# Kernel tuning notes

Hardware: AMD Instinct MI355X
Metric: run time of the kernel (lower is better)

Reference implementation:

```python
import jax, jax.numpy as jnp
import numpy as np

INV_TEMPERATURE = 0.125  # 1/sqrt(head_dim=64)


def setup_inputs() -> dict:
    key = jax.random.key(0)
    kq, kk, kv, kp, km = jax.random.split(key, 5)
    B, H, S, D = 8, 8, 2048, 64
    q = jax.random.normal(kq, (B, H, S, D), dtype=jnp.float32)
    k = jax.random.normal(kk, (B, H, S, D), dtype=jnp.float32)
    v = jax.random.normal(kv, (B, H, S, D), dtype=jnp.float32)
    pos_scores = jax.random.normal(kp, (1, H, S, S), dtype=jnp.float32)
    mask = jax.random.uniform(km, (1, 1, S, S), dtype=jnp.float32)
    return {"q": q, "k": k, "v": v, "pos_scores": pos_scores, "mask": mask}


def reference(q, k, v, pos_scores, mask):
    # sim = (q k^T) * inv_temp + pos_scores, then multiplicative mask
    sim = jnp.einsum('bhid,bhjd->bhij', q, k) * INV_TEMPERATURE
    sim = mask * (sim + pos_scores)
    attn = jax.nn.softmax(sim, axis=-1)
    out = jnp.einsum('bhij,bhjd->bhid', attn, v)
    return out
```

## Files before the change

### kernel.cpp

```cpp
#include <hip/hip_runtime.h>

constexpr int SEQ = 2048;
constexpr int HD  = 64;
constexpr int NH  = 8;
constexpr int NB  = 8;
constexpr int BM  = 64;
constexpr int BN  = 64;
constexpr int KST = 72;
constexpr float INV_T = 0.125f;
constexpr float LOG2E = 1.4426950408889634f;

typedef __attribute__((ext_vector_type(8))) short bf16x8;
typedef __attribute__((ext_vector_type(8))) short s16x8;
typedef __attribute__((ext_vector_type(4))) short s16x4;
typedef __attribute__((ext_vector_type(4))) float f32x4;
typedef __attribute__((ext_vector_type(4))) unsigned u32x4;

__device__ __forceinline__ short f2bf(float f) {
  unsigned u = __builtin_bit_cast(unsigned, f);
  u += 0x7fffu + ((u >> 16) & 1u);
  return (short)(u >> 16);
}
__device__ __forceinline__ float bf2f(short s) {
  unsigned u = ((unsigned)(unsigned short)s) << 16;
  return __builtin_bit_cast(float, u);
}
__device__ __forceinline__ float fast_exp2(float x) {
#if __has_builtin(__builtin_amdgcn_exp2f)
  return __builtin_amdgcn_exp2f(x);
#else
  return exp2f(x);
#endif
}

__global__ __launch_bounds__(256)
void prep_kv(const float* __restrict__ k, const float* __restrict__ v,
             unsigned short* __restrict__ kb, unsigned short* __restrict__ vt)
{
  __shared__ unsigned short t[HD * KST];
  const int bh = blockIdx.y, jt = blockIdx.x, tid = threadIdx.x;
  const size_t base = (size_t)bh * SEQ * HD + (size_t)jt * BN * HD;

  {
    const float* kp = k + base + 16 * tid;
    unsigned short ko[16];
    for (int e = 0; e < 4; ++e) {
      f32x4 x = *(const f32x4*)(kp + 4 * e);
      for (int c = 0; c < 4; ++c) ko[4 * e + c] = (unsigned short)f2bf(x[c]);
    }
    *(s16x8*)(kb + base + 16 * tid)     = *(const s16x8*)&ko[0];
    *(s16x8*)(kb + base + 16 * tid + 8) = *(const s16x8*)&ko[8];
  }
  {
    const float* vp = v + base + 16 * tid;
    const int j = tid >> 2, d0 = (tid & 3) * 16;
    for (int e = 0; e < 4; ++e) {
      f32x4 x = *(const f32x4*)(vp + 4 * e);
      for (int c = 0; c < 4; ++c) t[(d0 + 4 * e + c) * KST + j] = (unsigned short)f2bf(x[c]);
    }
  }
  __syncthreads();
  {
    const int d = tid >> 2, ch = tid & 3;
    const size_t ob = (size_t)bh * HD * SEQ + (size_t)d * SEQ + jt * BN + ch * 16;
    *(s16x8*)(vt + ob)     = *(const s16x8*)&t[d * KST + ch * 16];
    *(s16x8*)(vt + ob + 8) = *(const s16x8*)&t[d * KST + ch * 16 + 8];
  }
}

__global__ __launch_bounds__(256)
void prep_pack(const float* __restrict__ pos, const float* __restrict__ mask,
               unsigned* __restrict__ pk)
{
  const int w  = blockIdx.x * 256 + threadIdx.x;
  const int lq = w & 15;
  const int i  = (w >> 4) & 2047;
  const int jh = w >> 15;
  const int jt = jh & 31, h = jh >> 5;
  u32x4 o;
  for (int sub = 0; sub < 4; ++sub) {
    const int j = jt * 64 + sub * 16 + lq;
    float m = mask[(size_t)i * SEQ + j];
    float p = pos[((size_t)h * SEQ + i) * SEQ + j];
    unsigned mb = (unsigned)(unsigned short)f2bf(m * LOG2E);
    unsigned pb = (unsigned)(unsigned short)f2bf(m * p * LOG2E);
    o[sub] = (mb << 16) | pb;
  }
  *(u32x4*)(pk + (size_t)4 * w) = o;
}

__global__ __launch_bounds__(256, 8)
void attn_main(const float* __restrict__ q, const unsigned short* __restrict__ kb,
               const unsigned short* __restrict__ vt, const unsigned* __restrict__ pk,
               float* __restrict__ out)
{
  __shared__ unsigned short lds_k[BN * KST];
  __shared__ unsigned short lds_v[HD * KST];

  const int bh = blockIdx.y, h = bh & (NH - 1);
  const int i0 = blockIdx.x * BM;
  const int tid = threadIdx.x, wave = tid >> 6, lane = tid & 63;
  const int quad = lane >> 4, lq = lane & 15;

  bf16x8 aq[2];
  {
    const float* qp = q + ((size_t)bh * SEQ + i0 + wave * 16 + lq) * HD + quad * 8;
    for (int k0 = 0; k0 < 2; ++k0) {
      f32x4 x = *(const f32x4*)(qp + k0 * 32);
      f32x4 y = *(const f32x4*)(qp + k0 * 32 + 4);
      for (int c = 0; c < 4; ++c) {
        aq[k0][c]     = f2bf(x[c] * INV_T);
        aq[k0][4 + c] = f2bf(y[c] * INV_T);
      }
    }
  }

  f32x4 oacc[4];
  for (int d = 0; d < 4; ++d) oacc[d] = (f32x4){0.f, 0.f, 0.f, 0.f};
  float lrun[4] = {0.f, 0.f, 0.f, 0.f};

  const int lw = (tid >> 3) * KST + (tid & 7) * 8;
  const unsigned short* kgb = kb + (size_t)bh * SEQ * HD + 8 * tid;
  const unsigned short* vgb = vt + (size_t)bh * HD * SEQ + (tid >> 3) * SEQ + (tid & 7) * 8;
  const unsigned* mpb = pk + ((((size_t)h * 32) * SEQ + (i0 + wave * 16 + quad * 4)) * 16 + lq) * 4;

  for (int jt = 0; jt < SEQ / BN; ++jt) {
    __syncthreads();
    s16x8 kx0 = *(const s16x8*)(kgb + jt * 4096);
    s16x8 kx1 = *(const s16x8*)(kgb + jt * 4096 + 2048);
    s16x8 vx0 = *(const s16x8*)(vgb + jt * 64);
    s16x8 vx1 = *(const s16x8*)(vgb + jt * 64 + 32 * SEQ);
    *(s16x8*)&lds_k[lw]            = kx0;
    *(s16x8*)&lds_k[lw + 32 * KST] = kx1;
    *(s16x8*)&lds_v[lw]            = vx0;
    *(s16x8*)&lds_v[lw + 32 * KST] = vx1;
    __syncthreads();

    f32x4 sa[4];
    for (int s = 0; s < 4; ++s) sa[s] = (f32x4){0.f, 0.f, 0.f, 0.f};
    for (int k0 = 0; k0 < 2; ++k0)
      for (int s = 0; s < 4; ++s) {
        bf16x8 bk = *(const bf16x8*)&lds_k[(s * 16 + lq) * KST + k0 * 32 + quad * 8];
        sa[s] = __builtin_amdgcn_mfma_f32_16x16x32_bf16(aq[k0], bk, sa[s], 0, 0, 0);
      }
    __syncthreads();

    const unsigned* mp = mpb + (size_t)jt * (SEQ * 64);
    for (int r = 0; r < 4; ++r) {
      u32x4 u = *(const u32x4*)(mp + r * 64);
      float ps = 0.f;
      for (int s = 0; s < 4; ++s) {
        float mf = __builtin_bit_cast(float, u[s] & 0xffff0000u);
        float mq = __builtin_bit_cast(float, u[s] << 16);
        float p  = fast_exp2(fmaf(mf, sa[s][r], mq));
        unsigned pu = __builtin_bit_cast(unsigned, p);
        lds_k[wave * (16 * KST) + (quad * 4 + r) * KST + s * 16 + lq] = (unsigned short)(pu >> 16);
        ps += __builtin_bit_cast(float, pu & 0xffff0000u);
      }
      for (int off = 1; off < 16; off <<= 1) ps += __shfl_xor(ps, off);
      lrun[r] += ps;
    }
    asm volatile("s_waitcnt lgkmcnt(0)" ::: "memory");

    for (int k0 = 0; k0 < 2; ++k0) {
      bf16x8 ap = *(const bf16x8*)&lds_k[wave * (16 * KST) + lq * KST + k0 * 32 + quad * 8];
      for (int d = 0; d < 4; ++d) {
        bf16x8 bv = *(const bf16x8*)&lds_v[(d * 16 + lq) * KST + k0 * 32 + quad * 8];
        oacc[d] = __builtin_amdgcn_mfma_f32_16x16x32_bf16(ap, bv, oacc[d], 0, 0, 0);
      }
    }
  }

  for (int r = 0; r < 4; ++r) {
    const float inv = 1.0f / lrun[r];
    float* orow = out + ((size_t)bh * SEQ + i0 + wave * 16 + quad * 4 + r) * HD + lq;
    for (int d = 0; d < 4; ++d) orow[d * 16] = oacc[d][r] * inv;
  }
}

__global__ __launch_bounds__(256, 2)
void attn_fused(const float* __restrict__ q, const float* __restrict__ kk,
                const float* __restrict__ vv, const float* __restrict__ pos,
                const float* __restrict__ mask, float* __restrict__ out)
{
  __shared__ short lds_k[BN * KST];
  __shared__ short lds_v[HD * KST];
  __shared__ short lds_p[4][16 * KST];
  const int bh = blockIdx.y, h = bh & (NH - 1);
  const int i0 = blockIdx.x * BM;
  const int tid = threadIdx.x, wave = tid >> 6, lane = tid & 63;
  const int quad = lane >> 4, lq = lane & 15;
  bf16x8 aq[2];
  {
    const float* qp = q + ((size_t)bh * SEQ + i0 + wave * 16 + lq) * HD + quad * 8;
    for (int k0 = 0; k0 < 2; ++k0) {
      f32x4 x = *(const f32x4*)(qp + k0 * 32);
      f32x4 y = *(const f32x4*)(qp + k0 * 32 + 4);
      for (int j = 0; j < 4; ++j) { aq[k0][j] = f2bf(x[j] * INV_T); aq[k0][4 + j] = f2bf(y[j] * INV_T); }
    }
  }
  f32x4 oacc[4];
  for (int d = 0; d < 4; ++d) oacc[d] = (f32x4){0.f, 0.f, 0.f, 0.f};
  float mrun[4] = {-INFINITY, -INFINITY, -INFINITY, -INFINITY};
  float lrun[4] = {0.f, 0.f, 0.f, 0.f};
  const size_t kvbase = (size_t)bh * SEQ * HD;
  for (int jt = 0; jt < SEQ / BN; ++jt) {
    const int j0 = jt * BN;
    __syncthreads();
    for (int e = 0; e < 4; ++e) {
      int idx = e * 256 + tid, j = idx >> 4, d4 = (idx & 15) << 2;
      f32x4 kf = *(const f32x4*)(kk + kvbase + (size_t)(j0 + j) * HD + d4);
      s16x4 ks;
      for (int c = 0; c < 4; ++c) ks[c] = f2bf(kf[c]);
      *(s16x4*)&lds_k[j * KST + d4] = ks;
      f32x4 vf = *(const f32x4*)(vv + kvbase + (size_t)(j0 + j) * HD + d4);
      for (int c = 0; c < 4; ++c) lds_v[(d4 + c) * KST + j] = f2bf(vf[c]);
    }
    __syncthreads();
    float mk[4][4], pz[4][4];
    for (int r = 0; r < 4; ++r) {
      const int i = i0 + wave * 16 + quad * 4 + r;
      const float* mrow = mask + (size_t)i * SEQ + j0 + lq;
      const float* prow = pos + ((size_t)h * SEQ + i) * SEQ + j0 + lq;
      for (int s = 0; s < 4; ++s) { mk[r][s] = mrow[s * 16]; pz[r][s] = prow[s * 16]; }
    }
    f32x4 sa[4];
    for (int s = 0; s < 4; ++s) sa[s] = (f32x4){0.f, 0.f, 0.f, 0.f};
    for (int k0 = 0; k0 < 2; ++k0)
      for (int s = 0; s < 4; ++s) {
        bf16x8 bk = *(const bf16x8*)&lds_k[(s * 16 + lq) * KST + k0 * 32 + quad * 8];
        sa[s] = __builtin_amdgcn_mfma_f32_16x16x32_bf16(aq[k0], bk, sa[s], 0, 0, 0);
      }
    for (int r = 0; r < 4; ++r) {
      float s0 = mk[r][0] * (sa[0][r] + pz[r][0]);
      float s1 = mk[r][1] * (sa[1][r] + pz[r][1]);
      float s2 = mk[r][2] * (sa[2][r] + pz[r][2]);
      float s3 = mk[r][3] * (sa[3][r] + pz[r][3]);
      float rm = fmaxf(fmaxf(s0, s1), fmaxf(s2, s3));
      for (int off = 1; off < 16; off <<= 1) rm = fmaxf(rm, __shfl_xor(rm, off));
      float mn = fmaxf(mrun[r], rm);
      float al = __expf(mrun[r] - mn);
      mrun[r] = mn;
      short p0 = f2bf(__expf(s0 - mn)), p1 = f2bf(__expf(s1 - mn));
      short p2 = f2bf(__expf(s2 - mn)), p3 = f2bf(__expf(s3 - mn));
      float ps = bf2f(p0) + bf2f(p1) + bf2f(p2) + bf2f(p3);
      for (int off = 1; off < 16; off <<= 1) ps += __shfl_xor(ps, off);
      lrun[r] = lrun[r] * al + ps;
      for (int d = 0; d < 4; ++d) oacc[d][r] *= al;
      short* pr = &lds_p[wave][(quad * 4 + r) * KST + lq];
      pr[0] = p0; pr[16] = p1; pr[32] = p2; pr[48] = p3;
    }
    asm volatile("s_waitcnt lgkmcnt(0)" ::: "memory");
    for (int k0 = 0; k0 < 2; ++k0) {
      bf16x8 ap = *(const bf16x8*)&lds_p[wave][lq * KST + k0 * 32 + quad * 8];
      for (int d = 0; d < 4; ++d) {
        bf16x8 bv = *(const bf16x8*)&lds_v[(d * 16 + lq) * KST + k0 * 32 + quad * 8];
        oacc[d] = __builtin_amdgcn_mfma_f32_16x16x32_bf16(ap, bv, oacc[d], 0, 0, 0);
      }
    }
  }
  for (int r = 0; r < 4; ++r) {
    const int i = i0 + wave * 16 + quad * 4 + r;
    const float inv = 1.0f / lrun[r];
    float* orow = out + ((size_t)bh * SEQ + i) * HD + lq;
    for (int d = 0; d < 4; ++d) orow[d * 16] = oacc[d][r] * inv;
  }
}

extern "C" void kernel_launch(void* const* d_in, const int* in_sizes, int n_in,
                              void* d_out, int out_size, void* d_ws, size_t ws_size,
                              hipStream_t stream) {
  const float* q    = (const float*)d_in[0];
  const float* k    = (const float*)d_in[1];
  const float* v    = (const float*)d_in[2];
  const float* pos  = (const float*)d_in[3];
  const float* mask = (const float*)d_in[4];
  float* out = (float*)d_out;

  const size_t kv_elems = (size_t)NB * NH * SEQ * HD;
  const size_t kb_bytes = kv_elems * 2;
  const size_t pk_dwords = (size_t)NH * SEQ * SEQ;
  const size_t need = 2 * kb_bytes + pk_dwords * 4;

  if (ws_size >= need) {
    unsigned short* kb = (unsigned short*)d_ws;
    unsigned short* vt = (unsigned short*)((char*)d_ws + kb_bytes);
    unsigned*       pk = (unsigned*)((char*)d_ws + 2 * kb_bytes);
    prep_kv<<<dim3(SEQ / BN, NB * NH), dim3(256), 0, stream>>>(k, v, kb, vt);
    prep_pack<<<dim3((int)(pk_dwords / 4 / 256)), dim3(256), 0, stream>>>(pos, mask, pk);
    attn_main<<<dim3(SEQ / BM, NB * NH), dim3(256), 0, stream>>>(q, kb, vt, pk, out);
  } else {
    attn_fused<<<dim3(SEQ / BM, NB * NH), dim3(256), 0, stream>>>(q, k, v, pos, mask, out);
  }
}
```

Before: 497.7 us.

## Fuse pos/mask packing into attention kernel with batch-grouped block swizzle

Removes the separate prep_pack pass and reads fp32 pos_scores and mask directly inside attn_main. A 1D grid is swizzled so the 8 batches sharing the same head and row tile run close together and can reuse pos and mask from L2. The QK MFMA operands are swapped to transpose the score layout, so each lane holds one row and the per-row sum reduction moves out of the loop to a single final shuffle. In exchange, the main loop now reads four-byte fp32 values twice instead of one packed dword and depends on the L2 reuse that the swizzle sets up.

```diff
diff --git a/kernel.cpp b/kernel.cpp
--- a/kernel.cpp
+++ b/kernel.cpp
@@ -14,7 +14,6 @@
 typedef __attribute__((ext_vector_type(8))) short s16x8;
 typedef __attribute__((ext_vector_type(4))) short s16x4;
 typedef __attribute__((ext_vector_type(4))) float f32x4;
-typedef __attribute__((ext_vector_type(4))) unsigned u32x4;
 
 __device__ __forceinline__ short f2bf(float f) {
   unsigned u = __builtin_bit_cast(unsigned, f);
@@ -68,37 +67,22 @@
   }
 }
 
-__global__ __launch_bounds__(256)
-void prep_pack(const float* __restrict__ pos, const float* __restrict__ mask,
-               unsigned* __restrict__ pk)
-{
-  const int w  = blockIdx.x * 256 + threadIdx.x;
-  const int lq = w & 15;
-  const int i  = (w >> 4) & 2047;
-  const int jh = w >> 15;
-  const int jt = jh & 31, h = jh >> 5;
-  u32x4 o;
-  for (int sub = 0; sub < 4; ++sub) {
-    const int j = jt * 64 + sub * 16 + lq;
-    float m = mask[(size_t)i * SEQ + j];
-    float p = pos[((size_t)h * SEQ + i) * SEQ + j];
-    unsigned mb = (unsigned)(unsigned short)f2bf(m * LOG2E);
-    unsigned pb = (unsigned)(unsigned short)f2bf(m * p * LOG2E);
-    o[sub] = (mb << 16) | pb;
-  }
-  *(u32x4*)(pk + (size_t)4 * w) = o;
-}
-
 __global__ __launch_bounds__(256, 8)
 void attn_main(const float* __restrict__ q, const unsigned short* __restrict__ kb,
-               const unsigned short* __restrict__ vt, const unsigned* __restrict__ pk,
+               const unsigned short* __restrict__ vt,
+               const float* __restrict__ pos, const float* __restrict__ mask,
                float* __restrict__ out)
 {
   __shared__ unsigned short lds_k[BN * KST];
   __shared__ unsigned short lds_v[HD * KST];
 
-  const int bh = blockIdx.y, h = bh & (NH - 1);
-  const int i0 = blockIdx.x * BM;
+  const int n = blockIdx.x;
+  const int x = n & 7, b = (n >> 3) & 7, G = n >> 6;
+  const int g = G * 8 + x;
+  const int h = g >> 5, it = g & 31;
+  const int bh = b * NH + h;
+  const int i0 = it * BM;
+
   const int tid = threadIdx.x, wave = tid >> 6, lane = tid & 63;
   const int quad = lane >> 4, lq = lane & 15;
 
@@ -106,23 +90,29 @@
   {
     const float* qp = q + ((size_t)bh * SEQ + i0 + wave * 16 + lq) * HD + quad * 8;
     for (int k0 = 0; k0 < 2; ++k0) {
-      f32x4 x = *(const f32x4*)(qp + k0 * 32);
-      f32x4 y = *(const f32x4*)(qp + k0 * 32 + 4);
+      f32x4 xv = *(const f32x4*)(qp + k0 * 32);
+      f32x4 yv = *(const f32x4*)(qp + k0 * 32 + 4);
       for (int c = 0; c < 4; ++c) {
-        aq[k0][c]     = f2bf(x[c] * INV_T);
-        aq[k0][4 + c] = f2bf(y[c] * INV_T);
+        aq[k0][c]     = f2bf(xv[c] * INV_T);
+        aq[k0][4 + c] = f2bf(yv[c] * INV_T);
       }
     }
   }
 
   f32x4 oacc[4];
   for (int d = 0; d < 4; ++d) oacc[d] = (f32x4){0.f, 0.f, 0.f, 0.f};
-  float lrun[4] = {0.f, 0.f, 0.f, 0.f};
+  float lrun = 0.f;
 
   const int lw = (tid >> 3) * KST + (tid & 7) * 8;
   const unsigned short* kgb = kb + (size_t)bh * SEQ * HD + 8 * tid;
   const unsigned short* vgb = vt + (size_t)bh * HD * SEQ + (tid >> 3) * SEQ + (tid & 7) * 8;
-  const unsigned* mpb = pk + ((((size_t)h * 32) * SEQ + (i0 + wave * 16 + quad * 4)) * 16 + lq) * 4;
+
+  const int irow = i0 + wave * 16 + lq;
+  const float* mrow = mask + (size_t)irow * SEQ + quad * 4;
+  const float* prow = pos + ((size_t)h * SEQ + irow) * SEQ + quad * 4;
+
+  unsigned short* lds_p = lds_k;
+  const int pbase = wave * (16 * KST);
 
   for (int jt = 0; jt < SEQ / BN; ++jt) {
     __syncthreads();
@@ -137,33 +127,43 @@
     __syncthreads();
 
     f32x4 sa[4];
+#pragma unroll
     for (int s = 0; s < 4; ++s) sa[s] = (f32x4){0.f, 0.f, 0.f, 0.f};
+#pragma unroll
     for (int k0 = 0; k0 < 2; ++k0)
+#pragma unroll
       for (int s = 0; s < 4; ++s) {
         bf16x8 bk = *(const bf16x8*)&lds_k[(s * 16 + lq) * KST + k0 * 32 + quad * 8];
-        sa[s] = __builtin_amdgcn_mfma_f32_16x16x32_bf16(aq[k0], bk, sa[s], 0, 0, 0);
-      }
-    __syncthreads();
-
-    const unsigned* mp = mpb + (size_t)jt * (SEQ * 64);
-    for (int r = 0; r < 4; ++r) {
-      u32x4 u = *(const u32x4*)(mp + r * 64);
+        sa[s] = __builtin_amdgcn_mfma_f32_16x16x32_bf16(bk, aq[k0], sa[s], 0, 0, 0);
+      }
+    __syncthreads();
+
+    const float* mj = mrow + jt * 64;
+    const float* pj = prow + jt * 64;
+#pragma unroll
+    for (int s = 0; s < 4; ++s) {
+      f32x4 m4 = *(const f32x4*)(mj + s * 16);
+      f32x4 p4 = *(const f32x4*)(pj + s * 16);
+      s16x4 pb;
       float ps = 0.f;
-      for (int s = 0; s < 4; ++s) {
-        float mf = __builtin_bit_cast(float, u[s] & 0xffff0000u);
-        float mq = __builtin_bit_cast(float, u[s] << 16);
-        float p  = fast_exp2(fmaf(mf, sa[s][r], mq));
+#pragma unroll
+      for (int r = 0; r < 4; ++r) {
+        float t = m4[r] * LOG2E;
+        float a = fmaf(t, sa[s][r], t * p4[r]);
+        float p = fast_exp2(a);
         unsigned pu = __builtin_bit_cast(unsigned, p);
-        lds_k[wave * (16 * KST) + (quad * 4 + r) * KST + s * 16 + lq] = (unsigned short)(pu >> 16);
+        pb[r] = (short)(pu >> 16);
         ps += __builtin_bit_cast(float, pu & 0xffff0000u);
       }
-      for (int off = 1; off < 16; off <<= 1) ps += __shfl_xor(ps, off);
-      lrun[r] += ps;
+      lrun += ps;
+      *(s16x4*)&lds_p[pbase + lq * KST + s * 16 + quad * 4] = pb;
     }
     asm volatile("s_waitcnt lgkmcnt(0)" ::: "memory");
 
-    for (int k0 = 0; k0 < 2; ++k0) {
-      bf16x8 ap = *(const bf16x8*)&lds_k[wave * (16 * KST) + lq * KST + k0 * 32 + quad * 8];
+#pragma unroll
+    for (int k0 = 0; k0 < 2; ++k0) {
+      bf16x8 ap = *(const bf16x8*)&lds_p[pbase + lq * KST + k0 * 32 + quad * 8];
+#pragma unroll
       for (int d = 0; d < 4; ++d) {
         bf16x8 bv = *(const bf16x8*)&lds_v[(d * 16 + lq) * KST + k0 * 32 + quad * 8];
         oacc[d] = __builtin_amdgcn_mfma_f32_16x16x32_bf16(ap, bv, oacc[d], 0, 0, 0);
@@ -171,9 +171,15 @@
     }
   }
 
+  lrun += __shfl_xor(lrun, 16);
+  lrun += __shfl_xor(lrun, 32);
+
+#pragma unroll
   for (int r = 0; r < 4; ++r) {
-    const float inv = 1.0f / lrun[r];
+    const float lv = __shfl(lrun, quad * 4 + r);
+    const float inv = 1.0f / lv;
     float* orow = out + ((size_t)bh * SEQ + i0 + wave * 16 + quad * 4 + r) * HD + lq;
+#pragma unroll
     for (int d = 0; d < 4; ++d) orow[d * 16] = oacc[d][r] * inv;
   }
 }
@@ -194,9 +200,9 @@
   {
     const float* qp = q + ((size_t)bh * SEQ + i0 + wave * 16 + lq) * HD + quad * 8;
     for (int k0 = 0; k0 < 2; ++k0) {
-      f32x4 x = *(const f32x4*)(qp + k0 * 32);
-      f32x4 y = *(const f32x4*)(qp + k0 * 32 + 4);
-      for (int j = 0; j < 4; ++j) { aq[k0][j] = f2bf(x[j] * INV_T); aq[k0][4 + j] = f2bf(y[j] * INV_T); }
+      f32x4 xv = *(const f32x4*)(qp + k0 * 32);
+      f32x4 yv = *(const f32x4*)(qp + k0 * 32 + 4);
+      for (int j = 0; j < 4; ++j) { aq[k0][j] = f2bf(xv[j] * INV_T); aq[k0][4 + j] = f2bf(yv[j] * INV_T); }
     }
   }
   f32x4 oacc[4];
@@ -279,16 +285,13 @@
 
   const size_t kv_elems = (size_t)NB * NH * SEQ * HD;
   const size_t kb_bytes = kv_elems * 2;
-  const size_t pk_dwords = (size_t)NH * SEQ * SEQ;
-  const size_t need = 2 * kb_bytes + pk_dwords * 4;
+  const size_t need = 2 * kb_bytes;
 
   if (ws_size >= need) {
     unsigned short* kb = (unsigned short*)d_ws;
     unsigned short* vt = (unsigned short*)((char*)d_ws + kb_bytes);
-    unsigned*       pk = (unsigned*)((char*)d_ws + 2 * kb_bytes);
     prep_kv<<<dim3(SEQ / BN, NB * NH), dim3(256), 0, stream>>>(k, v, kb, vt);
-    prep_pack<<<dim3((int)(pk_dwords / 4 / 256)), dim3(256), 0, stream>>>(pos, mask, pk);
-    attn_main<<<dim3(SEQ / BM, NB * NH), dim3(256), 0, stream>>>(q, kb, vt, pk, out);
+    attn_main<<<dim3(NB * NH * SEQ / BM), dim3(256), 0, stream>>>(q, kb, vt, pos, mask, out);
   } else {
     attn_fused<<<dim3(SEQ / BM, NB * NH), dim3(256), 0, stream>>>(q, k, v, pos, mask, out);
   }
```

After: 567.4 us. 1.14x slower.
